# Kernel tuning notes

Hardware: AMD Instinct MI355X
Metric: run time of the kernel (lower is better)

## Reference

```python
import jax, jax.numpy as jnp
import numpy as np

K, D, N, T, B = 8, 16, 32, 200, 2048
_LOG2PI = float(np.log(2.0 * np.pi))


def setup_inputs() -> dict:
    key = jax.random.key(0)
    ks = jax.random.split(key, 13)
    return {
        "discrete_states": jax.random.randint(ks[0], (B, T), 0, K),
        "continuous_states": jax.random.normal(ks[1], (B, T, D), dtype=jnp.float32),
        "obs": jax.random.normal(ks[2], (B, T, N), dtype=jnp.float32),
        "discrete_init_logits": jax.random.normal(ks[3], (K,), dtype=jnp.float32),
        "continuous_init_locs": jax.random.normal(ks[4], (K, D), dtype=jnp.float32),
        "continuous_init_log_scales": jax.random.normal(ks[5], (K, D), dtype=jnp.float32),
        "state_transition_logits": jax.random.normal(ks[6], (K, K), dtype=jnp.float32),
        "dynamics_matrices": jax.random.normal(ks[7], (K, D, D), dtype=jnp.float32) * 0.3,
        "dynamics_offsets": jax.random.normal(ks[8], (K, D), dtype=jnp.float32),
        # NOTE: original code uses dynamics_log_scales directly as a scale (missing .exp());
        # we keep that math faithfully but init it strictly positive to stay finite.
        "dynamics_log_scales": jax.random.uniform(ks[9], (K, D), minval=0.5, maxval=1.5, dtype=jnp.float32),
        "emission_matrices": jax.random.normal(ks[10], (K, N, D), dtype=jnp.float32),
        "emission_offsets": jax.random.normal(ks[11], (K, N), dtype=jnp.float32),
        "emission_log_scales": jax.random.normal(ks[12], (K, N), dtype=jnp.float32),
    }


def _normal_lp(x, loc, scale):
    # elementwise Normal log-prob
    return -0.5 * jnp.square((x - loc) / scale) - jnp.log(scale) - 0.5 * _LOG2PI


def reference(discrete_states, continuous_states, obs,
              discrete_init_logits, continuous_init_locs, continuous_init_log_scales,
              state_transition_logits, dynamics_matrices, dynamics_offsets,
              dynamics_log_scales, emission_matrices, emission_offsets,
              emission_log_scales):
    """log p(s_{1:T}, z_{1:T}, x_{1:T}) -> [B]"""
    s0 = discrete_states[:, 0]                      # [B]
    z0 = continuous_states[:, 0]                    # [B,D]
    # p(s_1)
    lp = jax.nn.log_softmax(discrete_init_logits)[s0]
    # p(z_1 | s_1)
    lp = lp + _normal_lp(z0, continuous_init_locs[s0],
                         jnp.exp(continuous_init_log_scales[s0])).sum(-1)
    # p(s_t | s_{t-1}) for t=2..T, fully vectorized over time
    s_prev = discrete_states[:, :-1]
    s_cur = discrete_states[:, 1:]
    trans = jax.nn.log_softmax(state_transition_logits, axis=-1)  # [K,K]
    lp = lp + trans[s_prev, s_cur].sum(-1)
    # p(z_t | z_{t-1}, s_t)
    A = dynamics_matrices[s_cur]                    # [B,T-1,D,D] gather
    dyn_loc = jnp.einsum('btij,btj->bti', A, continuous_states[:, :-1]) + dynamics_offsets[s_cur]
    dyn_scale = dynamics_log_scales[s_cur]          # faithful: original omits .exp()
    lp = lp + _normal_lp(continuous_states[:, 1:], dyn_loc, dyn_scale).sum((-1, -2))
    # p(x_t | z_t, s_t) for all t
    C = emission_matrices[discrete_states]          # [B,T,N,D] gather
    em_loc = jnp.einsum('btij,btj->bti', C, continuous_states) + emission_offsets[discrete_states]
    em_scale = jnp.exp(emission_log_scales[discrete_states])
    lp = lp + _normal_lp(obs, em_loc, em_scale).sum((-1, -2))
    return lp
```

## Files before the change

### kernel.cpp

```cpp
#include <hip/hip_runtime.h>

#define KK 8
#define DD 16
#define NN 32
#define TT 200
#define BB 2048

#define SCU 260
#define SAU 132
#define SE 36
#define SD 20

#define WS_CU    0
#define WS_AU    2048
#define WS_EMOFF 3072
#define WS_EMINV 3328
#define WS_DYOFF 3584
#define WS_DYINV 3712
#define WS_INLOC 3840
#define WS_ININV 3968
#define WS_TRANS 4096
#define WS_EMC   4160
#define WS_DYC   4168
#define WS_INLP  4176

typedef __bf16 bf16x2 __attribute__((ext_vector_type(2)));

__device__ __forceinline__ float bflo(unsigned u) { return __uint_as_float(u << 16); }
__device__ __forceinline__ float bfhi(unsigned u) { return __uint_as_float(u & 0xffff0000u); }

__device__ __forceinline__ unsigned bfr(float f) {
  unsigned u = __float_as_uint(f);
  return (u + 0x7fffu + ((u >> 16) & 1u)) >> 16;
}
__device__ __forceinline__ unsigned bfpack(float f0, float f1) {
  return bfr(f0) | (bfr(f1) << 16);
}

__device__ __forceinline__ float dot2bf(unsigned a, unsigned b, float c) {
#if __has_builtin(__builtin_amdgcn_fdot2_bf16_bf16_f32)
  return __builtin_amdgcn_fdot2_bf16_bf16_f32(
      __builtin_bit_cast(bf16x2, a), __builtin_bit_cast(bf16x2, b), c);
#else
  float r = fmaf(bflo(a), bflo(b), c);
  return fmaf(bfhi(a), bfhi(b), r);
#endif
}

__device__ __forceinline__ float dot16d2(const unsigned* __restrict__ row,
                                         const unsigned* __restrict__ zp) {
  uint4 w0 = *reinterpret_cast<const uint4*>(row);
  uint4 w1 = *reinterpret_cast<const uint4*>(row + 4);
  float a = dot2bf(w0.x, zp[0], 0.f);
  float b = dot2bf(w0.y, zp[1], 0.f);
  a = dot2bf(w0.z, zp[2], a);
  b = dot2bf(w0.w, zp[3], b);
  a = dot2bf(w1.x, zp[4], a);
  b = dot2bf(w1.y, zp[5], b);
  a = dot2bf(w1.z, zp[6], a);
  b = dot2bf(w1.w, zp[7], b);
  return a + b;
}

__global__ __launch_bounds__(256) void prep_kernel(
    const float* __restrict__ initlg, const float* __restrict__ initloc,
    const float* __restrict__ initls, const float* __restrict__ transg,
    const float* __restrict__ Ag, const float* __restrict__ dynoff,
    const float* __restrict__ dynls, const float* __restrict__ Cg,
    const float* __restrict__ emoff, const float* __restrict__ emls,
    unsigned* __restrict__ ws, float* __restrict__ out) {
  const float HALF_LOG2PI = 0.91893853320467274178f;
  const int tid = threadIdx.x;
  float* wsf = reinterpret_cast<float*>(ws);

  for (int i = tid; i < 2048; i += 256)
    ws[WS_CU + i] = bfpack(Cg[2 * i], Cg[2 * i + 1]);
  for (int i = tid; i < 1024; i += 256)
    ws[WS_AU + i] = bfpack(Ag[2 * i], Ag[2 * i + 1]);
  if (tid < 256) { wsf[WS_EMOFF + tid] = emoff[tid]; wsf[WS_EMINV + tid] = expf(-emls[tid]); }
  if (tid < 128) {
    wsf[WS_DYOFF + tid] = dynoff[tid];
    wsf[WS_DYINV + tid] = 1.0f / dynls[tid];
    wsf[WS_INLOC + tid] = initloc[tid];
    wsf[WS_ININV + tid] = expf(-initls[tid]);
  }
  if (tid < 64) {
    int kr = tid >> 3;
    float mx = transg[kr * KK];
    for (int j = 1; j < KK; ++j) mx = fmaxf(mx, transg[kr * KK + j]);
    float ss = 0.f;
    for (int j = 0; j < KK; ++j) ss += expf(transg[kr * KK + j] - mx);
    wsf[WS_TRANS + tid] = transg[tid] - (logf(ss) + mx);
  }
  if (tid < 8) {
    int k = tid;
    float se = 0.f;
    for (int n = 0; n < NN; ++n) se -= emls[k * NN + n];
    wsf[WS_EMC + k] = se - NN * HALF_LOG2PI;
    float sd = 0.f;
    for (int d = 0; d < DD; ++d) sd -= logf(dynls[k * DD + d]);
    wsf[WS_DYC + k] = sd - DD * HALF_LOG2PI;
    float mx = initlg[0];
    for (int j = 1; j < KK; ++j) mx = fmaxf(mx, initlg[j]);
    float ss = 0.f;
    for (int j = 0; j < KK; ++j) ss += expf(initlg[j] - mx);
    float si = 0.f;
    for (int d = 0; d < DD; ++d) si -= initls[k * DD + d];
    wsf[WS_INLP + k] = initlg[k] - (logf(ss) + mx) + si - DD * HALF_LOG2PI;
  }
  for (int i = tid; i < BB; i += 256) out[i] = 0.f;
}

__global__ __launch_bounds__(256) void slds_lp_kernel(
    const int* __restrict__ dsts,
    const float* __restrict__ zg,
    const float* __restrict__ obsg,
    const unsigned* __restrict__ ws,
    float* __restrict__ out)
{
  __shared__ __align__(16) unsigned sCu[KK * SCU];
  __shared__ __align__(16) unsigned sAu[KK * SAU];
  __shared__ __align__(16) float sEmOff[KK * SE];
  __shared__ __align__(16) float sEmInv[KK * SE];
  __shared__ __align__(16) float sDynOff[KK * SD];
  __shared__ __align__(16) float sDynInv[KK * SD];
  __shared__ __align__(16) float sInitLoc[KK * SD];
  __shared__ __align__(16) float sInitInv[KK * SD];
  __shared__ float sTrans[KK * KK];
  __shared__ float sEmConst[KK];
  __shared__ float sDynConst[KK];
  __shared__ float sInitLp[KK];

  const int tid = threadIdx.x;
  const float* wsf = reinterpret_cast<const float*>(ws);

  for (int i = tid; i < 2048; i += 256) {
    int k = i >> 8, r = i & 255;
    sCu[k * SCU + r] = ws[WS_CU + i];
  }
  for (int i = tid; i < 1024; i += 256) {
    int k = i >> 7, r = i & 127;
    sAu[k * SAU + r] = ws[WS_AU + i];
  }
  if (tid < 256) {
    int k = tid >> 5, n = tid & 31;
    sEmOff[k * SE + n] = wsf[WS_EMOFF + tid];
    sEmInv[k * SE + n] = wsf[WS_EMINV + tid];
  }
  if (tid < 128) {
    int k = tid >> 4, d = tid & 15;
    sDynOff[k * SD + d] = wsf[WS_DYOFF + tid];
    sDynInv[k * SD + d] = wsf[WS_DYINV + tid];
    sInitLoc[k * SD + d] = wsf[WS_INLOC + tid];
    sInitInv[k * SD + d] = wsf[WS_ININV + tid];
  }
  if (tid < 64) sTrans[tid] = wsf[WS_TRANS + tid];
  if (tid < 8) {
    sEmConst[tid] = wsf[WS_EMC + tid];
    sDynConst[tid] = wsf[WS_DYC + tid];
    sInitLp[tid] = wsf[WS_INLP + tid];
  }
  __syncthreads();

  const int nItems = BB * TT;
  const int gstride = gridDim.x * blockDim.x;
  for (int item = blockIdx.x * blockDim.x + tid; item < nItems; item += gstride) {
    const int b = item / TT;
    const int t = item - b * TT;
    const int lane = tid & 63;

    float zz[16];
    unsigned zzp[8];
    {
      const float4* p = reinterpret_cast<const float4*>(zg + (size_t)item * DD);
      float4 a0 = p[0], a1 = p[1], a2 = p[2], a3 = p[3];
      zz[0] = a0.x; zz[1] = a0.y; zz[2] = a0.z; zz[3] = a0.w;
      zz[4] = a1.x; zz[5] = a1.y; zz[6] = a1.z; zz[7] = a1.w;
      zz[8] = a2.x; zz[9] = a2.y; zz[10] = a2.z; zz[11] = a2.w;
      zz[12] = a3.x; zz[13] = a3.y; zz[14] = a3.z; zz[15] = a3.w;
#pragma unroll
      for (int i = 0; i < 8; ++i) zzp[i] = bfpack(zz[2 * i], zz[2 * i + 1]);
    }
    const int s = dsts[item];

    unsigned zpp[8];
    int sp = __shfl_up(s, 1, 64);
#pragma unroll
    for (int i = 0; i < 8; ++i) zpp[i] = __shfl_up(zzp[i], 1, 64);
    if (lane == 0 && t != 0) {
      sp = dsts[item - 1];
      const float4* p = reinterpret_cast<const float4*>(zg + (size_t)(item - 1) * DD);
      float4 a0 = p[0], a1 = p[1], a2 = p[2], a3 = p[3];
      zpp[0] = bfpack(a0.x, a0.y); zpp[1] = bfpack(a0.z, a0.w);
      zpp[2] = bfpack(a1.x, a1.y); zpp[3] = bfpack(a1.z, a1.w);
      zpp[4] = bfpack(a2.x, a2.y); zpp[5] = bfpack(a2.z, a2.w);
      zpp[6] = bfpack(a3.x, a3.y); zpp[7] = bfpack(a3.z, a3.w);
    }

    const float4* o4 = reinterpret_cast<const float4*>(obsg + (size_t)item * NN);
    const int cb = s * SCU;
    const int eb4 = s * (SE / 4);
    float4 oa = o4[0], ob = o4[1];
    float acc = 0.f;
#pragma unroll 1
    for (int gg = 0; gg < 4; ++gg) {
      float4 na = oa, nb = ob;
      if (gg < 3) { na = o4[2 * gg + 2]; nb = o4[2 * gg + 3]; }
#pragma unroll
      for (int h = 0; h < 2; ++h) {
        const int g = 2 * gg + h;
        float4 o = h ? ob : oa;
        float4 off = reinterpret_cast<const float4*>(sEmOff)[eb4 + g];
        float4 inv = reinterpret_cast<const float4*>(sEmInv)[eb4 + g];
        int n0 = g * 4;
        float l0 = dot16d2(&sCu[cb + (n0 + 0) * 8], zzp) + off.x;
        float l1 = dot16d2(&sCu[cb + (n0 + 1) * 8], zzp) + off.y;
        float l2 = dot16d2(&sCu[cb + (n0 + 2) * 8], zzp) + off.z;
        float l3 = dot16d2(&sCu[cb + (n0 + 3) * 8], zzp) + off.w;
        float d0 = (o.x - l0) * inv.x;
        float d1 = (o.y - l1) * inv.y;
        float d2 = (o.z - l2) * inv.z;
        float d3 = (o.w - l3) * inv.w;
        acc = fmaf(d0, d0, acc); acc = fmaf(d1, d1, acc);
        acc = fmaf(d2, d2, acc); acc = fmaf(d3, d3, acc);
      }
      oa = na; ob = nb;
    }
    float lp = -0.5f * acc + sEmConst[s];

    if (t != 0) {
      const int ab = s * SAU;
      const int db4 = s * (SD / 4);
      float a2acc = 0.f;
#pragma unroll 2
      for (int g = 0; g < 4; ++g) {
        float4 off = reinterpret_cast<const float4*>(sDynOff)[db4 + g];
        float4 inv = reinterpret_cast<const float4*>(sDynInv)[db4 + g];
        int i0 = g * 4;
        float l0 = dot16d2(&sAu[ab + (i0 + 0) * 8], zpp) + off.x;
        float l1 = dot16d2(&sAu[ab + (i0 + 1) * 8], zpp) + off.y;
        float l2 = dot16d2(&sAu[ab + (i0 + 2) * 8], zpp) + off.z;
        float l3 = dot16d2(&sAu[ab + (i0 + 3) * 8], zpp) + off.w;
        float d0 = (zz[i0 + 0] - l0) * inv.x;
        float d1 = (zz[i0 + 1] - l1) * inv.y;
        float d2 = (zz[i0 + 2] - l2) * inv.z;
        float d3 = (zz[i0 + 3] - l3) * inv.w;
        a2acc = fmaf(d0, d0, a2acc); a2acc = fmaf(d1, d1, a2acc);
        a2acc = fmaf(d2, d2, a2acc); a2acc = fmaf(d3, d3, a2acc);
      }
      lp += -0.5f * a2acc + sDynConst[s] + sTrans[sp * KK + s];
    } else {
      const int ib4 = s * (SD / 4);
      float a2acc = 0.f;
#pragma unroll 2
      for (int g = 0; g < 4; ++g) {
        float4 loc = reinterpret_cast<const float4*>(sInitLoc)[ib4 + g];
        float4 inv = reinterpret_cast<const float4*>(sInitInv)[ib4 + g];
        int i0 = g * 4;
        float d0 = (zz[i0 + 0] - loc.x) * inv.x;
        float d1 = (zz[i0 + 1] - loc.y) * inv.y;
        float d2 = (zz[i0 + 2] - loc.z) * inv.z;
        float d3 = (zz[i0 + 3] - loc.w) * inv.w;
        a2acc = fmaf(d0, d0, a2acc); a2acc = fmaf(d1, d1, a2acc);
        a2acc = fmaf(d2, d2, a2acc); a2acc = fmaf(d3, d3, a2acc);
      }
      lp += -0.5f * a2acc + sInitLp[s];
    }

    float v = lp;
#pragma unroll
    for (int off = 1; off < 64; off <<= 1) {
      float ov = __shfl_up(v, off, 64);
      if (t >= off && lane >= off) v += ov;
    }
    if (lane == 63 || t == TT - 1) atomicAdd(&out[b], v);
  }
}

extern "C" void kernel_launch(void* const* d_in, const int* in_sizes, int n_in,
                              void* d_out, int out_size, void* d_ws, size_t ws_size,
                              hipStream_t stream) {
  const int*   dsts    = (const int*)d_in[0];
  const float* zg      = (const float*)d_in[1];
  const float* obsg    = (const float*)d_in[2];
  const float* initlg  = (const float*)d_in[3];
  const float* initloc = (const float*)d_in[4];
  const float* initls  = (const float*)d_in[5];
  const float* transg  = (const float*)d_in[6];
  const float* Ag      = (const float*)d_in[7];
  const float* dynoff  = (const float*)d_in[8];
  const float* dynls   = (const float*)d_in[9];
  const float* Cg      = (const float*)d_in[10];
  const float* emoff   = (const float*)d_in[11];
  const float* emls    = (const float*)d_in[12];
  float* out = (float*)d_out;
  unsigned* ws = (unsigned*)d_ws;

  prep_kernel<<<1, 256, 0, stream>>>(initlg, initloc, initls, transg, Ag,
                                     dynoff, dynls, Cg, emoff, emls, ws, out);
  slds_lp_kernel<<<1600, 256, 0, stream>>>(dsts, zg, obsg, ws, out);
}
```

Baseline: 146.5 us.

## Process two consecutive timesteps per thread and drop grid-stride loop

Each thread now handles two adjacent (b,t) items, so the second item's dynamics term reuses the first item's packed state from registers instead of a cross-lane shuffle. Loads of states, observations and discrete indices are widened. The grid-stride loop is removed and the grid halved to exactly cover all items, and the segmented scan is adjusted for the pair granularity. This roughly doubles register use per thread and halves the number of threads, which may reduce occupancy.

```diff
diff --git a/kernel.cpp b/kernel.cpp
--- a/kernel.cpp
+++ b/kernel.cpp
@@ -162,119 +162,149 @@
   }
   __syncthreads();
 
-  const int nItems = BB * TT;
-  const int gstride = gridDim.x * blockDim.x;
-  for (int item = blockIdx.x * blockDim.x + tid; item < nItems; item += gstride) {
-    const int b = item / TT;
-    const int t = item - b * TT;
-    const int lane = tid & 63;
-
-    float zz[16];
-    unsigned zzp[8];
-    {
-      const float4* p = reinterpret_cast<const float4*>(zg + (size_t)item * DD);
-      float4 a0 = p[0], a1 = p[1], a2 = p[2], a3 = p[3];
-      zz[0] = a0.x; zz[1] = a0.y; zz[2] = a0.z; zz[3] = a0.w;
-      zz[4] = a1.x; zz[5] = a1.y; zz[6] = a1.z; zz[7] = a1.w;
-      zz[8] = a2.x; zz[9] = a2.y; zz[10] = a2.z; zz[11] = a2.w;
-      zz[12] = a3.x; zz[13] = a3.y; zz[14] = a3.z; zz[15] = a3.w;
+  const int j = blockIdx.x * 256 + tid;
+  const int item0 = 2 * j;
+  const int b = item0 / TT;
+  const int t0 = item0 - b * TT;
+  const int lane = tid & 63;
+
+  int2 ss = *reinterpret_cast<const int2*>(dsts + item0);
+  const int s0 = ss.x, s1 = ss.y;
+
+  float zz0[16], zz1[16];
+  unsigned zzp0[8], zzp1[8];
+  {
+    const float4* p = reinterpret_cast<const float4*>(zg + (size_t)item0 * DD);
+    float4 a0 = p[0], a1 = p[1], a2 = p[2], a3 = p[3];
+    zz0[0] = a0.x; zz0[1] = a0.y; zz0[2] = a0.z; zz0[3] = a0.w;
+    zz0[4] = a1.x; zz0[5] = a1.y; zz0[6] = a1.z; zz0[7] = a1.w;
+    zz0[8] = a2.x; zz0[9] = a2.y; zz0[10] = a2.z; zz0[11] = a2.w;
+    zz0[12] = a3.x; zz0[13] = a3.y; zz0[14] = a3.z; zz0[15] = a3.w;
+    float4 b0 = p[4], b1 = p[5], b2 = p[6], b3 = p[7];
+    zz1[0] = b0.x; zz1[1] = b0.y; zz1[2] = b0.z; zz1[3] = b0.w;
+    zz1[4] = b1.x; zz1[5] = b1.y; zz1[6] = b1.z; zz1[7] = b1.w;
+    zz1[8] = b2.x; zz1[9] = b2.y; zz1[10] = b2.z; zz1[11] = b2.w;
+    zz1[12] = b3.x; zz1[13] = b3.y; zz1[14] = b3.z; zz1[15] = b3.w;
 #pragma unroll
-      for (int i = 0; i < 8; ++i) zzp[i] = bfpack(zz[2 * i], zz[2 * i + 1]);
+    for (int i = 0; i < 8; ++i) {
+      zzp0[i] = bfpack(zz0[2 * i], zz0[2 * i + 1]);
+      zzp1[i] = bfpack(zz1[2 * i], zz1[2 * i + 1]);
     }
-    const int s = dsts[item];
-
-    unsigned zpp[8];
-    int sp = __shfl_up(s, 1, 64);
+  }
+
+  unsigned zpp0[8];
+  int sp0 = __shfl_up(s1, 1, 64);
 #pragma unroll
-    for (int i = 0; i < 8; ++i) zpp[i] = __shfl_up(zzp[i], 1, 64);
-    if (lane == 0 && t != 0) {
-      sp = dsts[item - 1];
-      const float4* p = reinterpret_cast<const float4*>(zg + (size_t)(item - 1) * DD);
-      float4 a0 = p[0], a1 = p[1], a2 = p[2], a3 = p[3];
-      zpp[0] = bfpack(a0.x, a0.y); zpp[1] = bfpack(a0.z, a0.w);
-      zpp[2] = bfpack(a1.x, a1.y); zpp[3] = bfpack(a1.z, a1.w);
-      zpp[4] = bfpack(a2.x, a2.y); zpp[5] = bfpack(a2.z, a2.w);
-      zpp[6] = bfpack(a3.x, a3.y); zpp[7] = bfpack(a3.z, a3.w);
+  for (int i = 0; i < 8; ++i) zpp0[i] = __shfl_up(zzp1[i], 1, 64);
+  if (lane == 0 && t0 != 0) {
+    sp0 = dsts[item0 - 1];
+    const float4* p = reinterpret_cast<const float4*>(zg + (size_t)(item0 - 1) * DD);
+    float4 a0 = p[0], a1 = p[1], a2 = p[2], a3 = p[3];
+    zpp0[0] = bfpack(a0.x, a0.y); zpp0[1] = bfpack(a0.z, a0.w);
+    zpp0[2] = bfpack(a1.x, a1.y); zpp0[3] = bfpack(a1.z, a1.w);
+    zpp0[4] = bfpack(a2.x, a2.y); zpp0[5] = bfpack(a2.z, a2.w);
+    zpp0[6] = bfpack(a3.x, a3.y); zpp0[7] = bfpack(a3.z, a3.w);
+  }
+
+  const float4* o4a = reinterpret_cast<const float4*>(obsg + (size_t)item0 * NN);
+  const float4* o4b = o4a + (NN / 4);
+  const int cb0 = s0 * SCU, eb0 = s0 * (SE / 4);
+  const int cb1 = s1 * SCU, eb1 = s1 * (SE / 4);
+  float accA = 0.f, accB = 0.f;
+#pragma unroll 2
+  for (int g = 0; g < 8; ++g) {
+    const int n0 = g * 4;
+    float4 oA = o4a[g];
+    float4 oB = o4b[g];
+    float4 offA = reinterpret_cast<const float4*>(sEmOff)[eb0 + g];
+    float4 invA = reinterpret_cast<const float4*>(sEmInv)[eb0 + g];
+    float la0 = dot16d2(&sCu[cb0 + (n0 + 0) * 8], zzp0) + offA.x;
+    float la1 = dot16d2(&sCu[cb0 + (n0 + 1) * 8], zzp0) + offA.y;
+    float la2 = dot16d2(&sCu[cb0 + (n0 + 2) * 8], zzp0) + offA.z;
+    float la3 = dot16d2(&sCu[cb0 + (n0 + 3) * 8], zzp0) + offA.w;
+    float4 offB = reinterpret_cast<const float4*>(sEmOff)[eb1 + g];
+    float4 invB = reinterpret_cast<const float4*>(sEmInv)[eb1 + g];
+    float lb0 = dot16d2(&sCu[cb1 + (n0 + 0) * 8], zzp1) + offB.x;
+    float lb1 = dot16d2(&sCu[cb1 + (n0 + 1) * 8], zzp1) + offB.y;
+    float lb2 = dot16d2(&sCu[cb1 + (n0 + 2) * 8], zzp1) + offB.z;
+    float lb3 = dot16d2(&sCu[cb1 + (n0 + 3) * 8], zzp1) + offB.w;
+    float e0 = (oA.x - la0) * invA.x, e1 = (oA.y - la1) * invA.y;
+    float e2 = (oA.z - la2) * invA.z, e3 = (oA.w - la3) * invA.w;
+    accA = fmaf(e0, e0, accA); accA = fmaf(e1, e1, accA);
+    accA = fmaf(e2, e2, accA); accA = fmaf(e3, e3, accA);
+    float f0 = (oB.x - lb0) * invB.x, f1 = (oB.y - lb1) * invB.y;
+    float f2 = (oB.z - lb2) * invB.z, f3 = (oB.w - lb3) * invB.w;
+    accB = fmaf(f0, f0, accB); accB = fmaf(f1, f1, accB);
+    accB = fmaf(f2, f2, accB); accB = fmaf(f3, f3, accB);
+  }
+  float lp = -0.5f * (accA + accB) + sEmConst[s0] + sEmConst[s1];
+
+  {
+    const int ab1 = s1 * SAU, db1 = s1 * (SD / 4);
+    float dacc = 0.f;
+#pragma unroll 2
+    for (int g = 0; g < 4; ++g) {
+      float4 off = reinterpret_cast<const float4*>(sDynOff)[db1 + g];
+      float4 inv = reinterpret_cast<const float4*>(sDynInv)[db1 + g];
+      int i0 = g * 4;
+      float l0 = dot16d2(&sAu[ab1 + (i0 + 0) * 8], zzp0) + off.x;
+      float l1 = dot16d2(&sAu[ab1 + (i0 + 1) * 8], zzp0) + off.y;
+      float l2 = dot16d2(&sAu[ab1 + (i0 + 2) * 8], zzp0) + off.z;
+      float l3 = dot16d2(&sAu[ab1 + (i0 + 3) * 8], zzp0) + off.w;
+      float d0 = (zz1[i0 + 0] - l0) * inv.x;
+      float d1 = (zz1[i0 + 1] - l1) * inv.y;
+      float d2 = (zz1[i0 + 2] - l2) * inv.z;
+      float d3 = (zz1[i0 + 3] - l3) * inv.w;
+      dacc = fmaf(d0, d0, dacc); dacc = fmaf(d1, d1, dacc);
+      dacc = fmaf(d2, d2, dacc); dacc = fmaf(d3, d3, dacc);
     }
-
-    const float4* o4 = reinterpret_cast<const float4*>(obsg + (size_t)item * NN);
-    const int cb = s * SCU;
-    const int eb4 = s * (SE / 4);
-    float4 oa = o4[0], ob = o4[1];
-    float acc = 0.f;
-#pragma unroll 1
-    for (int gg = 0; gg < 4; ++gg) {
-      float4 na = oa, nb = ob;
-      if (gg < 3) { na = o4[2 * gg + 2]; nb = o4[2 * gg + 3]; }
+    lp += -0.5f * dacc + sDynConst[s1] + sTrans[s0 * KK + s1];
+  }
+  if (t0 != 0) {
+    const int ab0 = s0 * SAU, db0 = s0 * (SD / 4);
+    float dacc = 0.f;
+#pragma unroll 2
+    for (int g = 0; g < 4; ++g) {
+      float4 off = reinterpret_cast<const float4*>(sDynOff)[db0 + g];
+      float4 inv = reinterpret_cast<const float4*>(sDynInv)[db0 + g];
+      int i0 = g * 4;
+      float l0 = dot16d2(&sAu[ab0 + (i0 + 0) * 8], zpp0) + off.x;
+      float l1 = dot16d2(&sAu[ab0 + (i0 + 1) * 8], zpp0) + off.y;
+      float l2 = dot16d2(&sAu[ab0 + (i0 + 2) * 8], zpp0) + off.z;
+      float l3 = dot16d2(&sAu[ab0 + (i0 + 3) * 8], zpp0) + off.w;
+      float d0 = (zz0[i0 + 0] - l0) * inv.x;
+      float d1 = (zz0[i0 + 1] - l1) * inv.y;
+      float d2 = (zz0[i0 + 2] - l2) * inv.z;
+      float d3 = (zz0[i0 + 3] - l3) * inv.w;
+      dacc = fmaf(d0, d0, dacc); dacc = fmaf(d1, d1, dacc);
+      dacc = fmaf(d2, d2, dacc); dacc = fmaf(d3, d3, dacc);
+    }
+    lp += -0.5f * dacc + sDynConst[s0] + sTrans[sp0 * KK + s0];
+  } else {
+    const int ib0 = s0 * (SD / 4);
+    float dacc = 0.f;
+#pragma unroll 2
+    for (int g = 0; g < 4; ++g) {
+      float4 loc = reinterpret_cast<const float4*>(sInitLoc)[ib0 + g];
+      float4 inv = reinterpret_cast<const float4*>(sInitInv)[ib0 + g];
+      int i0 = g * 4;
+      float d0 = (zz0[i0 + 0] - loc.x) * inv.x;
+      float d1 = (zz0[i0 + 1] - loc.y) * inv.y;
+      float d2 = (zz0[i0 + 2] - loc.z) * inv.z;
+      float d3 = (zz0[i0 + 3] - loc.w) * inv.w;
+      dacc = fmaf(d0, d0, dacc); dacc = fmaf(d1, d1, dacc);
+      dacc = fmaf(d2, d2, dacc); dacc = fmaf(d3, d3, dacc);
+    }
+    lp += -0.5f * dacc + sInitLp[s0];
+  }
+
+  float v = lp;
 #pragma unroll
-      for (int h = 0; h < 2; ++h) {
-        const int g = 2 * gg + h;
-        float4 o = h ? ob : oa;
-        float4 off = reinterpret_cast<const float4*>(sEmOff)[eb4 + g];
-        float4 inv = reinterpret_cast<const float4*>(sEmInv)[eb4 + g];
-        int n0 = g * 4;
-        float l0 = dot16d2(&sCu[cb + (n0 + 0) * 8], zzp) + off.x;
-        float l1 = dot16d2(&sCu[cb + (n0 + 1) * 8], zzp) + off.y;
-        float l2 = dot16d2(&sCu[cb + (n0 + 2) * 8], zzp) + off.z;
-        float l3 = dot16d2(&sCu[cb + (n0 + 3) * 8], zzp) + off.w;
-        float d0 = (o.x - l0) * inv.x;
-        float d1 = (o.y - l1) * inv.y;
-        float d2 = (o.z - l2) * inv.z;
-        float d3 = (o.w - l3) * inv.w;
-        acc = fmaf(d0, d0, acc); acc = fmaf(d1, d1, acc);
-        acc = fmaf(d2, d2, acc); acc = fmaf(d3, d3, acc);
-      }
-      oa = na; ob = nb;
-    }
-    float lp = -0.5f * acc + sEmConst[s];
-
-    if (t != 0) {
-      const int ab = s * SAU;
-      const int db4 = s * (SD / 4);
-      float a2acc = 0.f;
-#pragma unroll 2
-      for (int g = 0; g < 4; ++g) {
-        float4 off = reinterpret_cast<const float4*>(sDynOff)[db4 + g];
-        float4 inv = reinterpret_cast<const float4*>(sDynInv)[db4 + g];
-        int i0 = g * 4;
-        float l0 = dot16d2(&sAu[ab + (i0 + 0) * 8], zpp) + off.x;
-        float l1 = dot16d2(&sAu[ab + (i0 + 1) * 8], zpp) + off.y;
-        float l2 = dot16d2(&sAu[ab + (i0 + 2) * 8], zpp) + off.z;
-        float l3 = dot16d2(&sAu[ab + (i0 + 3) * 8], zpp) + off.w;
-        float d0 = (zz[i0 + 0] - l0) * inv.x;
-        float d1 = (zz[i0 + 1] - l1) * inv.y;
-        float d2 = (zz[i0 + 2] - l2) * inv.z;
-        float d3 = (zz[i0 + 3] - l3) * inv.w;
-        a2acc = fmaf(d0, d0, a2acc); a2acc = fmaf(d1, d1, a2acc);
-        a2acc = fmaf(d2, d2, a2acc); a2acc = fmaf(d3, d3, a2acc);
-      }
-      lp += -0.5f * a2acc + sDynConst[s] + sTrans[sp * KK + s];
-    } else {
-      const int ib4 = s * (SD / 4);
-      float a2acc = 0.f;
-#pragma unroll 2
-      for (int g = 0; g < 4; ++g) {
-        float4 loc = reinterpret_cast<const float4*>(sInitLoc)[ib4 + g];
-        float4 inv = reinterpret_cast<const float4*>(sInitInv)[ib4 + g];
-        int i0 = g * 4;
-        float d0 = (zz[i0 + 0] - loc.x) * inv.x;
-        float d1 = (zz[i0 + 1] - loc.y) * inv.y;
-        float d2 = (zz[i0 + 2] - loc.z) * inv.z;
-        float d3 = (zz[i0 + 3] - loc.w) * inv.w;
-        a2acc = fmaf(d0, d0, a2acc); a2acc = fmaf(d1, d1, a2acc);
-        a2acc = fmaf(d2, d2, a2acc); a2acc = fmaf(d3, d3, a2acc);
-      }
-      lp += -0.5f * a2acc + sInitLp[s];
-    }
-
-    float v = lp;
-#pragma unroll
-    for (int off = 1; off < 64; off <<= 1) {
-      float ov = __shfl_up(v, off, 64);
-      if (t >= off && lane >= off) v += ov;
-    }
-    if (lane == 63 || t == TT - 1) atomicAdd(&out[b], v);
-  }
+  for (int off = 1; off < 64; off <<= 1) {
+    float ov = __shfl_up(v, off, 64);
+    if (t0 >= 2 * off && lane >= off) v += ov;
+  }
+  if (lane == 63 || t0 == TT - 2) atomicAdd(&out[b], v);
 }
 
 extern "C" void kernel_launch(void* const* d_in, const int* in_sizes, int n_in,
@@ -298,5 +328,5 @@
 
   prep_kernel<<<1, 256, 0, stream>>>(initlg, initloc, initls, transg, Ag,
                                      dynoff, dynls, Cg, emoff, emls, ws, out);
-  slds_lp_kernel<<<1600, 256, 0, stream>>>(dsts, zg, obsg, ws, out);
-}
+  slds_lp_kernel<<<800, 256, 0, stream>>>(dsts, zg, obsg, ws, out);
+}
```

Measured after the change: 151.4 us. 3.4% more time.
